# Kernel tuning notes

Hardware: AMD Instinct MI355X
Metric: run time of the kernel (lower is better)

The kernel has to match this reference:

```python
import jax, jax.numpy as jnp
import numpy as np

B, N, K, D, V, L = 16, 512, 16, 256, 64, 2


def setup_inputs() -> dict:
    key = jax.random.key(0)
    ks = jax.random.split(key, 20)
    inp = {
        "node_reps": jax.random.normal(ks[0], (B, N, D), dtype=jnp.float32),
        "mask": jax.random.uniform(ks[1], (B, N), dtype=jnp.float32),
        "in_indices": jax.random.randint(ks[2], (B, N, K), 0, N),
        "in_edges": jax.random.randint(ks[3], (B, N, K), 0, V),
        "in_mask": jax.random.uniform(ks[4], (B, N, K), dtype=jnp.float32),
        "out_indices": jax.random.randint(ks[5], (B, N, K), 0, N),
        "out_edges": jax.random.randint(ks[6], (B, N, K), 0, V),
        "out_mask": jax.random.uniform(ks[7], (B, N, K), dtype=jnp.float32),
        "edge_emb": jax.random.normal(ks[8], (V, D), dtype=jnp.float32) * 0.02,
        # packed gate weights, order [ig, fg, og, cell] along last dim
        "Wi": jax.random.normal(ks[9], (2 * D, 4 * D), dtype=jnp.float32) * 0.02,
        "Wo": jax.random.normal(ks[10], (2 * D, 4 * D), dtype=jnp.float32) * 0.02,
        "Ui": jax.random.normal(ks[11], (2 * D, 4 * D), dtype=jnp.float32) * 0.02,
        "Uo": jax.random.normal(ks[12], (2 * D, 4 * D), dtype=jnp.float32) * 0.02,
        "bi": jnp.zeros((4 * D,), dtype=jnp.float32),
        "bo": jnp.zeros((4 * D,), dtype=jnp.float32),
        "bui": jnp.zeros((4 * D,), dtype=jnp.float32),
        "buo": jnp.zeros((4 * D,), dtype=jnp.float32),
    }
    return inp


def _agg(h, idx, edge_reps, nmask):
    # gather neighbor states: [B,N,K,D]
    neigh = h[jnp.arange(h.shape[0])[:, None, None], idx]
    x = jnp.concatenate([neigh, edge_reps], axis=-1) * nmask[..., None]
    return x.sum(axis=2)  # [B,N,2D]


def reference(node_reps, mask, in_indices, in_edges, in_mask,
              out_indices, out_edges, out_mask,
              edge_emb, Wi, Wo, Ui, Uo, bi, bo, bui, buo):
    in_edge_reps = edge_emb[in_edges]    # [B,N,K,D]
    out_edge_reps = edge_emb[out_edges]  # [B,N,K,D]

    in_reps = _agg(node_reps, in_indices, in_edge_reps, in_mask)     # [B,N,2D]
    out_reps = _agg(node_reps, out_indices, out_edge_reps, out_mask)  # [B,N,2D]
    z_static = in_reps @ Wi + bi + out_reps @ Wo + bo  # [B,N,4D]

    h = node_reps
    c = jnp.zeros_like(node_reps)
    reps = []
    for _ in range(L):
        in_pre = _agg(h, in_indices, in_edge_reps, in_mask)
        out_pre = _agg(h, out_indices, out_edge_reps, out_mask)
        z = z_static + in_pre @ Ui + bui + out_pre @ Uo + buo  # [B,N,4D]
        ig, fg, og, ci = jnp.split(z, 4, axis=-1)
        ig = jax.nn.sigmoid(ig)
        fg = jax.nn.sigmoid(fg)
        og = jax.nn.sigmoid(og)
        ci = jnp.tanh(ci)
        c_new = fg * c + ig * ci
        h_new = og * jnp.tanh(c_new)
        c = c_new * mask[..., None]
        h = h_new * mask[..., None]
        reps.append(h)
    return (jnp.stack(reps, axis=0), h, c)
```

## Files before the change

### kernel.cpp

```cpp
#include <hip/hip_runtime.h>
#include <math.h>

#define Kn 16
#define Dd 256
#define NC 1024
#define XS 640
#define MR 8192

typedef _Float16 h8 __attribute__((ext_vector_type(8)));
typedef _Float16 h4 __attribute__((ext_vector_type(4)));
typedef _Float16 h2 __attribute__((ext_vector_type(2)));
typedef float f4 __attribute__((ext_vector_type(4)));

__device__ __forceinline__ void gload16(_Float16* lds, const _Float16* g) {
  __builtin_amdgcn_global_load_lds(
      (const __attribute__((address_space(1))) void*)g,
      (__attribute__((address_space(3))) void*)lds, 16, 0, 0);
}

__device__ __forceinline__ float fsigm(float x) { return 1.f / (1.f + __expf(-x)); }
__device__ __forceinline__ float ftanh(float x) { return 2.f / (1.f + __expf(-2.f * x)) - 1.f; }

__global__ __launch_bounds__(256, 4) void mega2_kernel(
    const float* __restrict__ node_reps, const float* __restrict__ emb,
    const int* __restrict__ iidx, const float* __restrict__ im,
    const int* __restrict__ oidx, const float* __restrict__ om,
    const int* __restrict__ ie, const int* __restrict__ oe,
    const float* __restrict__ Wi, const float* __restrict__ Wo,
    const float* __restrict__ Ui, const float* __restrict__ Uo,
    const float* __restrict__ bi, const float* __restrict__ bo,
    const float* __restrict__ bui, const float* __restrict__ buo,
    _Float16* __restrict__ X, _Float16* __restrict__ W0f,
    _Float16* __restrict__ Wlf, float* __restrict__ biasq) {
  __shared__ __align__(16) char smem[20480];
  const int b = blockIdx.x, t = threadIdx.x;

  if (b < 2048) {
    const int lane = t & 63;
    const int wid = t >> 6;
    const int row = (b & 7) * 1024 + (b >> 3) * 4 + wid;
    const int half = lane >> 5;
    const int lc = lane & 31;
    const int sel = lane >> 4, p16 = lane & 15;

    const int bb = row * Kn + p16;
    const int* ap = (sel == 0)   ? (iidx + bb)
                    : (sel == 1) ? ((const int*)im + bb)
                    : (sel == 2) ? (oidx + bb)
                                 : ((const int*)om + bb);
    const int cmb = *ap;
    const int cmbe = *(((lane & 16) ? oe : ie) + bb);

    const int hb = row & ~511;
    const float* hp = node_reps + ((size_t)hb << 8) + (lc << 3);

    float acc[8] = {};
#pragma unroll
    for (int kb = 0; kb < 2; kb++) {
      f4 w0[8], w1[8];
#pragma unroll
      for (int k = 0; k < 8; k++) {
        const int ik = __shfl(cmb, (lane & 32) | (kb * 8 + k), 64);
        const float* p = hp + ((size_t)ik << 8);
        w0[k] = *(const f4*)p;
        w1[k] = *(const f4*)(p + 4);
      }
      __builtin_amdgcn_sched_barrier(0);
#pragma unroll
      for (int k = 0; k < 8; k++) {
        const float mk = __int_as_float(__shfl(cmb, (lane & 32) | 16 | (kb * 8 + k), 64));
#pragma unroll
        for (int c = 0; c < 4; c++) {
          acc[c] += mk * w0[k][c];
          acc[4 + c] += mk * w1[k][c];
        }
      }
    }

    {
      float b0 = 0.f, b1 = 0.f;
      const int vmine = 2 * lane - half * 64;
#pragma unroll
      for (int k = 0; k < 16; k++) {
        const int ec = __shfl(cmbe, (half << 4) | k, 64);
        const float mc = __int_as_float(__shfl(cmb, (lane & 32) | 16 | k, 64));
        b0 += (ec == vmine) ? mc : 0.f;
        b1 += (ec == vmine + 1) ? mc : 0.f;
      }
      h2 bp;
      bp[0] = (_Float16)b0;
      bp[1] = (_Float16)b1;
      *(h2*)&X[(size_t)row * XS + 512 + lane * 2] = bp;
    }

    h8 o;
#pragma unroll
    for (int c = 0; c < 8; c++) o[c] = (_Float16)acc[c];
    *(h8*)&X[(size_t)row * XS + half * 256 + lc * 8] = o;
  } else if (b < 2176) {
    float* seT = (float*)smem;
    float* sa = (float*)(smem + 4096);
    const int pb = b - 2048;
    const int vgrp = pb >> 2, cq = pb & 3;
    const int dir = vgrp >> 4;
    const int v0 = (vgrp & 15) * 4;
    const float* Wa = dir ? Wo : Wi;
    const float* Ua = dir ? Uo : Ui;
#pragma unroll
    for (int r = 0; r < 4; r++) seT[t * 4 + r] = emb[(v0 + r) * 256 + t];
    __syncthreads();

    const int l = t & 63, ds = t >> 6;
    const int cp0 = cq * 256 + l * 4;
    const int g = (cp0 >> 4) & 3;
    const int d0 = ((cp0 >> 6) << 4) + (cp0 & 15);
    const int c0 = g * 256 + d0;
    const float* wp = Wa + (size_t)(256 + ds * 64) * NC + c0;
    const float* up = Ua + (size_t)(256 + ds * 64) * NC + c0;
    const float* sT = seT + (ds * 64) * 4;

    f4 av[4] = {};
    for (int bb8 = 0; bb8 < 8; bb8++) {
      f4 wv8[8], uv8[8];
#pragma unroll
      for (int ii = 0; ii < 8; ii++) {
        const int dd = bb8 * 8 + ii;
        wv8[ii] = *(const f4*)(wp + (size_t)dd * NC);
        uv8[ii] = *(const f4*)(up + (size_t)dd * NC);
      }
      __builtin_amdgcn_sched_barrier(0);
#pragma unroll
      for (int ii = 0; ii < 8; ii++) {
        const int dd = bb8 * 8 + ii;
        const f4 wv = wv8[ii] + uv8[ii];
        const f4 s0 = *(const f4*)&sT[dd * 4];
        av[0] += s0[0] * wv;
        av[1] += s0[1] * wv;
        av[2] += s0[2] * wv;
        av[3] += s0[3] * wv;
      }
    }
#pragma unroll
    for (int r = 0; r < 4; r++) *(f4*)&sa[((ds * 4 + r) * 64 + l) * 4] = av[r];
    __syncthreads();
    {
      const int r = t >> 6, fl = t & 63;
      f4 s = {0.f, 0.f, 0.f, 0.f};
#pragma unroll
      for (int d = 0; d < 4; d++) s += *(const f4*)&sa[((d * 4 + r) * 64 + fl) * 4];
      const int vvg = vgrp * 4 + r;
      const int kt = 16 + (vvg >> 5);
      const int lhi = (vvg >> 3) & 3;
      const int j = vvg & 7;
      const int cpb = cq * 256 + fl * 4;
#pragma unroll
      for (int i = 0; i < 4; i++) {
        const int cp = cpb + i;
        W0f[kt * 32768 + (cp >> 4) * 512 + (lhi * 16 + (cp & 15)) * 8 + j] = (_Float16)s[i];
      }
    }
  } else if (b < 2208) {
    const int p = b - 2176;
    const int kk = t >> 3;
    const int tc = t & 7;
    const int k = (p & 15) * 32 + kk;
    const float* rowp;
    const float* rowp2 = nullptr;
    if (p < 16) {
      rowp  = (k < 256) ? Wi + (size_t)k * NC : Wo + (size_t)(k - 256) * NC;
      rowp2 = (k < 256) ? Ui + (size_t)k * NC : Uo + (size_t)(k - 256) * NC;
    } else {
      rowp  = (k < 256) ? Ui + (size_t)k * NC : Uo + (size_t)(k - 256) * NC;
    }
    _Float16* dst = (p < 16) ? (W0f + p * 32768) : (Wlf + (p - 16) * 32768);
    const int lane0 = (kk >> 3) * 16;
    const int j = kk & 7;
    for (int bb8 = 0; bb8 < 4; bb8++) {
      f4 w8[8], u8[8];
#pragma unroll
      for (int ii = 0; ii < 8; ii++) {
        const int c = (bb8 * 8 + ii) * 32 + tc * 4;
        w8[ii] = *(const f4*)(rowp + c);
        if (p < 16) u8[ii] = *(const f4*)(rowp2 + c);
      }
      __builtin_amdgcn_sched_barrier(0);
#pragma unroll
      for (int ii = 0; ii < 8; ii++) {
        const int c = (bb8 * 8 + ii) * 32 + tc * 4;
        const int g = c >> 8, d = c & 255;
        const int nt = 4 * (d >> 4) + g;
        const int lb = lane0 + (d & 15);
        f4 v = w8[ii];
        if (p < 16) v += u8[ii];
#pragma unroll
        for (int q = 0; q < 4; q++)
          dst[nt * 512 + (lb + q) * 8 + j] = (_Float16)v[q];
      }
    }
  } else {
#pragma unroll
    for (int i = 0; i < 4; i++) {
      const int cq = t * 4 + i;
      const int dd = cq >> 2, g = cq & 3;
      const int c = g * 256 + dd;
      biasq[cq] = bi[c] + bo[c] + bui[c] + buo[c];
    }
  }
}

__global__ __launch_bounds__(256, 4) void agg_kernel(
    const _Float16* __restrict__ src,
    const int* __restrict__ iidx, const float* __restrict__ im,
    const int* __restrict__ oidx, const float* __restrict__ om,
    _Float16* __restrict__ X) {
  const int lane = threadIdx.x & 63;
  const int wid = threadIdx.x >> 6;
  const int b = blockIdx.x;
  const int row = (b & 7) * 1024 + (b >> 3) * 4 + wid;
  const int half = lane >> 5;
  const int lc = lane & 31;
  const int sel = lane >> 4, p16 = lane & 15;

  const int bb = row * Kn + p16;
  const int* ap = (sel == 0)   ? (iidx + bb)
                  : (sel == 1) ? ((const int*)im + bb)
                  : (sel == 2) ? (oidx + bb)
                               : ((const int*)om + bb);
  const int cmb = *ap;

  const int hb = row & ~511;
  const _Float16* hp = src + ((size_t)hb << 8) + (lc << 3);
  _Float16* xp = &X[(size_t)row * XS + half * 256 + lc * 8];

  const h8 xold = *(const h8*)xp;

  h8 w[16];
#pragma unroll
  for (int k = 0; k < 16; k++) {
    const int ik = __shfl(cmb, (lane & 32) | k, 64);
    w[k] = *(const h8*)(hp + ((size_t)ik << 8));
  }
  __builtin_amdgcn_sched_barrier(0);

  float acc[8] = {};
#pragma unroll
  for (int k = 0; k < 16; k++) {
    const float mk = __int_as_float(__shfl(cmb, (lane & 32) | 16 | k, 64));
#pragma unroll
    for (int c = 0; c < 8; c++) acc[c] += mk * (float)w[k][c];
  }

  h8 o;
#pragma unroll
  for (int c = 0; c < 8; c++) o[c] = (_Float16)(acc[c] - (float)xold[c]);
  *(h8*)xp = o;
}

template <bool WITH_Z>
__global__ __launch_bounds__(512) void fused_gemm(
    const _Float16* __restrict__ A, const _Float16* __restrict__ Wf,
    const float* __restrict__ biasq, _Float16* __restrict__ zq,
    const float* __restrict__ mask,
    float* __restrict__ reps, float* __restrict__ hbuf,
    _Float16* __restrict__ h16, float* __restrict__ cbuf) {
  constexpr int KT = WITH_Z ? 20 : 16;
  constexpr int D = 2;
  __shared__ __align__(16) _Float16 lds[3][8192];

  const int wg = (blockIdx.x & 7) * 64 + (blockIdx.x >> 3);
  const int bm = wg >> 3, bn = wg & 7;
  const int tid = threadIdx.x, lane = tid & 63, wid = tid >> 6;
  const int wr = wid >> 1, wc = wid & 1;
  const int lr = lane & 15, lg = lane >> 4;

  f4 acc[2][4] = {};

  const _Float16* srcA0 = A + (size_t)(bm * 128 + wid * 16 + lr) * XS + lg * 8;
  const _Float16* srcB0 = Wf + ((size_t)bn * 8 + wid) * 512 + lane * 8;
  const int woff = wid * 512;

  auto stage = [&](int buf, int kt) {
    _Float16* base = lds[buf];
    gload16(base + woff, srcA0 + kt * 32);
    gload16(base + 4096 + woff, srcB0 + (size_t)kt * 32768);
  };

  stage(0, 0);
  stage(1, 1);
  asm volatile("s_waitcnt vmcnt(%0)" :: "i"(D) : "memory");
  __builtin_amdgcn_s_barrier();

  int cur = 0;
  for (int kt = 0; kt < KT; kt++) {
    if (kt + 2 < KT) stage(cur == 0 ? 2 : cur - 1, kt + 2);

    const _Float16* base = lds[cur];
    h8 a[2], bfr[4];
#pragma unroll
    for (int m = 0; m < 2; m++) a[m] = *(const h8*)&base[(wr * 2 + m) * 512 + lane * 8];
#pragma unroll
    for (int n = 0; n < 4; n++) bfr[n] = *(const h8*)&base[4096 + (wc * 4 + n) * 512 + lane * 8];
    asm volatile("s_waitcnt lgkmcnt(0)" ::: "memory");
    __builtin_amdgcn_sched_barrier(0);

    __builtin_amdgcn_s_setprio(1);
#pragma unroll
    for (int m = 0; m < 2; m++)
#pragma unroll
      for (int n = 0; n < 4; n++)
        acc[m][n] = __builtin_amdgcn_mfma_f32_16x16x32_f16(a[m], bfr[n], acc[m][n], 0, 0, 0);
    __builtin_amdgcn_s_setprio(0);

    if (kt + 2 < KT) asm volatile("s_waitcnt vmcnt(%0)" :: "i"(D) : "memory");
    else             asm volatile("s_waitcnt vmcnt(0)" ::: "memory");
    __builtin_amdgcn_sched_barrier(0);
    __builtin_amdgcn_s_barrier();

    cur = (cur == 2) ? 0 : cur + 1;
  }

  const int d = (bn * 2 + wc) * 16 + lr;
  const int row0 = bm * 128 + wr * 32;
  f4 bq = {0.f, 0.f, 0.f, 0.f};
  if (WITH_Z) bq = *(const f4*)&biasq[d * 4];
#pragma unroll
  for (int i = 0; i < 2; i++) {
#pragma unroll
    for (int r = 0; r < 4; r++) {
      const int row = row0 + i * 16 + lg * 4 + r;
      const size_t off = (size_t)row * Dd + d;
      const float mk = mask[row];
      float zi, zf, zo, zc, cold;
      if (WITH_Z) {
        zi = acc[i][0][r] + bq.x;
        zf = acc[i][1][r] + bq.y;
        zo = acc[i][2][r] + bq.z;
        zc = acc[i][3][r] + bq.w;
        h4 oz;
        oz[0] = (_Float16)zi; oz[1] = (_Float16)zf;
        oz[2] = (_Float16)zo; oz[3] = (_Float16)zc;
        *(h4*)&zq[off * 4] = oz;
        cold = 0.f;
      } else {
        const h4 zb = *(const h4*)&zq[off * 4];
        zi = (float)zb[0] + acc[i][0][r];
        zf = (float)zb[1] + acc[i][1][r];
        zo = (float)zb[2] + acc[i][2][r];
        zc = (float)zb[3] + acc[i][3][r];
        cold = fsigm((float)zb[0]) * ftanh((float)zb[3]) * mk;
      }
      const float ig = fsigm(zi), fg = fsigm(zf), og = fsigm(zo), ci = ftanh(zc);
      const float cn = fg * cold + ig * ci;
      const float hn = og * ftanh(cn);
      const float hm = hn * mk;
      if (WITH_Z) {
        __builtin_nontemporal_store(hm, &reps[off]);
        h16[off] = (_Float16)hm;
      } else {
        __builtin_nontemporal_store(hm, &reps[off]);
        __builtin_nontemporal_store(hm, &hbuf[off]);
        __builtin_nontemporal_store(cn * mk, &cbuf[off]);
      }
    }
  }
}

extern "C" void kernel_launch(void* const* d_in, const int* in_sizes, int n_in,
                              void* d_out, int out_size, void* d_ws, size_t ws_size,
                              hipStream_t stream) {
  const float* node_reps = (const float*)d_in[0];
  const float* mask      = (const float*)d_in[1];
  const int*   in_idx    = (const int*)d_in[2];
  const int*   in_edges  = (const int*)d_in[3];
  const float* in_mask   = (const float*)d_in[4];
  const int*   out_idx   = (const int*)d_in[5];
  const int*   out_edges = (const int*)d_in[6];
  const float* out_mask  = (const float*)d_in[7];
  const float* edge_emb  = (const float*)d_in[8];
  const float* Wi  = (const float*)d_in[9];
  const float* Wo  = (const float*)d_in[10];
  const float* Ui  = (const float*)d_in[11];
  const float* Uo  = (const float*)d_in[12];
  const float* bi  = (const float*)d_in[13];
  const float* bo  = (const float*)d_in[14];
  const float* bui = (const float*)d_in[15];
  const float* buo = (const float*)d_in[16];

  float* out = (float*)d_out;
  const size_t MD = (size_t)MR * Dd;
  float* reps0 = out;
  float* reps1 = out + MD;
  float* hbuf  = out + 2 * MD;
  float* cbuf  = out + 3 * MD;

  _Float16* X    = (_Float16*)d_ws;
  _Float16* zq   = X + (size_t)MR * XS;
  _Float16* W0f  = zq + (size_t)MR * NC;
  _Float16* Wlf  = W0f + 640 * 1024;
  _Float16* h16  = Wlf + 512 * 1024;
  float*    biasq = (float*)(h16 + (size_t)MR * Dd);

  mega2_kernel<<<2209, 256, 0, stream>>>(node_reps, edge_emb, in_idx, in_mask,
                                         out_idx, out_mask, in_edges, out_edges,
                                         Wi, Wo, Ui, Uo, bi, bo, bui, buo,
                                         X, W0f, Wlf, biasq);
  fused_gemm<true><<<512, 512, 0, stream>>>(
      X, W0f, biasq, zq, mask, reps0, nullptr, h16, nullptr);
  agg_kernel<<<2048, 256, 0, stream>>>(h16, in_idx, in_mask, out_idx, out_mask, X);
  fused_gemm<false><<<512, 512, 0, stream>>>(
      X, Wlf, nullptr, zq, mask, reps1, hbuf, nullptr, cbuf);
}
```

Baseline: 72.20 us.

## Convert node_reps to fp16 up front and split first aggregation into own kernel

The weight-packing work and an fp32-to-fp16 conversion of node_reps now run in a small prep kernel. The first-layer neighbor aggregation becomes a separate kernel that gathers fp16 rows, with all 16 neighbor loads issued at once. This halves the bytes read by the random-access gather, but adds one kernel launch, an extra full pass over node_reps, and a serialization point. Aggregation inputs are also rounded to fp16 before summation.

```diff
diff --git a/kernel.cpp b/kernel.cpp
--- a/kernel.cpp
+++ b/kernel.cpp
@@ -21,87 +21,21 @@
 __device__ __forceinline__ float fsigm(float x) { return 1.f / (1.f + __expf(-x)); }
 __device__ __forceinline__ float ftanh(float x) { return 2.f / (1.f + __expf(-2.f * x)) - 1.f; }
 
-__global__ __launch_bounds__(256, 4) void mega2_kernel(
+__global__ __launch_bounds__(256) void prep_kernel(
     const float* __restrict__ node_reps, const float* __restrict__ emb,
-    const int* __restrict__ iidx, const float* __restrict__ im,
-    const int* __restrict__ oidx, const float* __restrict__ om,
-    const int* __restrict__ ie, const int* __restrict__ oe,
     const float* __restrict__ Wi, const float* __restrict__ Wo,
     const float* __restrict__ Ui, const float* __restrict__ Uo,
     const float* __restrict__ bi, const float* __restrict__ bo,
     const float* __restrict__ bui, const float* __restrict__ buo,
-    _Float16* __restrict__ X, _Float16* __restrict__ W0f,
-    _Float16* __restrict__ Wlf, float* __restrict__ biasq) {
+    _Float16* __restrict__ W0f, _Float16* __restrict__ Wlf,
+    float* __restrict__ biasq, _Float16* __restrict__ n16) {
   __shared__ __align__(16) char smem[20480];
   const int b = blockIdx.x, t = threadIdx.x;
 
-  if (b < 2048) {
-    const int lane = t & 63;
-    const int wid = t >> 6;
-    const int row = (b & 7) * 1024 + (b >> 3) * 4 + wid;
-    const int half = lane >> 5;
-    const int lc = lane & 31;
-    const int sel = lane >> 4, p16 = lane & 15;
-
-    const int bb = row * Kn + p16;
-    const int* ap = (sel == 0)   ? (iidx + bb)
-                    : (sel == 1) ? ((const int*)im + bb)
-                    : (sel == 2) ? (oidx + bb)
-                                 : ((const int*)om + bb);
-    const int cmb = *ap;
-    const int cmbe = *(((lane & 16) ? oe : ie) + bb);
-
-    const int hb = row & ~511;
-    const float* hp = node_reps + ((size_t)hb << 8) + (lc << 3);
-
-    float acc[8] = {};
-#pragma unroll
-    for (int kb = 0; kb < 2; kb++) {
-      f4 w0[8], w1[8];
-#pragma unroll
-      for (int k = 0; k < 8; k++) {
-        const int ik = __shfl(cmb, (lane & 32) | (kb * 8 + k), 64);
-        const float* p = hp + ((size_t)ik << 8);
-        w0[k] = *(const f4*)p;
-        w1[k] = *(const f4*)(p + 4);
-      }
-      __builtin_amdgcn_sched_barrier(0);
-#pragma unroll
-      for (int k = 0; k < 8; k++) {
-        const float mk = __int_as_float(__shfl(cmb, (lane & 32) | 16 | (kb * 8 + k), 64));
-#pragma unroll
-        for (int c = 0; c < 4; c++) {
-          acc[c] += mk * w0[k][c];
-          acc[4 + c] += mk * w1[k][c];
-        }
-      }
-    }
-
-    {
-      float b0 = 0.f, b1 = 0.f;
-      const int vmine = 2 * lane - half * 64;
-#pragma unroll
-      for (int k = 0; k < 16; k++) {
-        const int ec = __shfl(cmbe, (half << 4) | k, 64);
-        const float mc = __int_as_float(__shfl(cmb, (lane & 32) | 16 | k, 64));
-        b0 += (ec == vmine) ? mc : 0.f;
-        b1 += (ec == vmine + 1) ? mc : 0.f;
-      }
-      h2 bp;
-      bp[0] = (_Float16)b0;
-      bp[1] = (_Float16)b1;
-      *(h2*)&X[(size_t)row * XS + 512 + lane * 2] = bp;
-    }
-
-    h8 o;
-#pragma unroll
-    for (int c = 0; c < 8; c++) o[c] = (_Float16)acc[c];
-    *(h8*)&X[(size_t)row * XS + half * 256 + lc * 8] = o;
-  } else if (b < 2176) {
+  if (b < 128) {
     float* seT = (float*)smem;
     float* sa = (float*)(smem + 4096);
-    const int pb = b - 2048;
-    const int vgrp = pb >> 2, cq = pb & 3;
+    const int vgrp = b >> 2, cq = b & 3;
     const int dir = vgrp >> 4;
     const int v0 = (vgrp & 15) * 4;
     const float* Wa = dir ? Wo : Wi;
@@ -159,8 +93,8 @@
         W0f[kt * 32768 + (cp >> 4) * 512 + (lhi * 16 + (cp & 15)) * 8 + j] = (_Float16)s[i];
       }
     }
-  } else if (b < 2208) {
-    const int p = b - 2176;
+  } else if (b < 160) {
+    const int p = b - 128;
     const int kk = t >> 3;
     const int tc = t & 7;
     const int k = (p & 15) * 32 + kk;
@@ -197,7 +131,7 @@
           dst[nt * 512 + (lb + q) * 8 + j] = (_Float16)v[q];
       }
     }
-  } else {
+  } else if (b == 160) {
 #pragma unroll
     for (int i = 0; i < 4; i++) {
       const int cq = t * 4 + i;
@@ -205,10 +139,85 @@
       const int c = g * 256 + dd;
       biasq[cq] = bi[c] + bo[c] + bui[c] + buo[c];
     }
-  }
-}
-
-__global__ __launch_bounds__(256, 4) void agg_kernel(
+  } else {
+    const int cb = b - 161;
+#pragma unroll
+    for (int r = 0; r < 8; r++) {
+      const int off = cb * 16384 + r * 2048 + t * 8;
+      const f4 v0 = *(const f4*)(node_reps + off);
+      const f4 v1 = *(const f4*)(node_reps + off + 4);
+      h8 o;
+#pragma unroll
+      for (int jj = 0; jj < 4; jj++) { o[jj] = (_Float16)v0[jj]; o[jj + 4] = (_Float16)v1[jj]; }
+      *(h8*)&n16[off] = o;
+    }
+  }
+}
+
+__global__ __launch_bounds__(256, 4) void agg0_kernel(
+    const _Float16* __restrict__ n16,
+    const int* __restrict__ iidx, const float* __restrict__ im,
+    const int* __restrict__ oidx, const float* __restrict__ om,
+    const int* __restrict__ ie, const int* __restrict__ oe,
+    _Float16* __restrict__ X) {
+  const int lane = threadIdx.x & 63;
+  const int wid = threadIdx.x >> 6;
+  const int b = blockIdx.x;
+  const int row = (b & 7) * 1024 + (b >> 3) * 4 + wid;
+  const int half = lane >> 5;
+  const int lc = lane & 31;
+  const int sel = lane >> 4, p16 = lane & 15;
+
+  const int bb = row * Kn + p16;
+  const int* ap = (sel == 0)   ? (iidx + bb)
+                  : (sel == 1) ? ((const int*)im + bb)
+                  : (sel == 2) ? (oidx + bb)
+                               : ((const int*)om + bb);
+  const int cmb = *ap;
+  const int cmbe = *(((lane & 16) ? oe : ie) + bb);
+
+  const int hb = row & ~511;
+  const _Float16* hp = n16 + ((size_t)hb << 8) + (lc << 3);
+
+  h8 w[16];
+#pragma unroll
+  for (int k = 0; k < 16; k++) {
+    const int ik = __shfl(cmb, (lane & 32) | k, 64);
+    w[k] = *(const h8*)(hp + ((size_t)ik << 8));
+  }
+  __builtin_amdgcn_sched_barrier(0);
+
+  float acc[8] = {};
+#pragma unroll
+  for (int k = 0; k < 16; k++) {
+    const float mk = __int_as_float(__shfl(cmb, (lane & 32) | 16 | k, 64));
+#pragma unroll
+    for (int c = 0; c < 8; c++) acc[c] += mk * (float)w[k][c];
+  }
+
+  {
+    float b0 = 0.f, b1 = 0.f;
+    const int vmine = 2 * lane - half * 64;
+#pragma unroll
+    for (int k = 0; k < 16; k++) {
+      const int ec = __shfl(cmbe, (half << 4) | k, 64);
+      const float mc = __int_as_float(__shfl(cmb, (lane & 32) | 16 | k, 64));
+      b0 += (ec == vmine) ? mc : 0.f;
+      b1 += (ec == vmine + 1) ? mc : 0.f;
+    }
+    h2 bp;
+    bp[0] = (_Float16)b0;
+    bp[1] = (_Float16)b1;
+    *(h2*)&X[(size_t)row * XS + 512 + lane * 2] = bp;
+  }
+
+  h8 o;
+#pragma unroll
+  for (int c = 0; c < 8; c++) o[c] = (_Float16)acc[c];
+  *(h8*)&X[(size_t)row * XS + half * 256 + lc * 8] = o;
+}
+
+__global__ __launch_bounds__(256, 4) void agg1_kernel(
     const _Float16* __restrict__ src,
     const int* __restrict__ iidx, const float* __restrict__ im,
     const int* __restrict__ oidx, const float* __restrict__ om,
@@ -397,16 +406,17 @@
   _Float16* zq   = X + (size_t)MR * XS;
   _Float16* W0f  = zq + (size_t)MR * NC;
   _Float16* Wlf  = W0f + 640 * 1024;
-  _Float16* h16  = Wlf + 512 * 1024;
+  _Float16* n16  = Wlf + 512 * 1024;
+  _Float16* h16  = n16 + (size_t)MR * Dd;
   float*    biasq = (float*)(h16 + (size_t)MR * Dd);
 
-  mega2_kernel<<<2209, 256, 0, stream>>>(node_reps, edge_emb, in_idx, in_mask,
-                                         out_idx, out_mask, in_edges, out_edges,
-                                         Wi, Wo, Ui, Uo, bi, bo, bui, buo,
-                                         X, W0f, Wlf, biasq);
+  prep_kernel<<<289, 256, 0, stream>>>(node_reps, edge_emb, Wi, Wo, Ui, Uo,
+                                       bi, bo, bui, buo, W0f, Wlf, biasq, n16);
+  agg0_kernel<<<2048, 256, 0, stream>>>(n16, in_idx, in_mask, out_idx, out_mask,
+                                        in_edges, out_edges, X);
   fused_gemm<true><<<512, 512, 0, stream>>>(
       X, W0f, biasq, zq, mask, reps0, nullptr, h16, nullptr);
-  agg_kernel<<<2048, 256, 0, stream>>>(h16, in_idx, in_mask, out_idx, out_mask, X);
+  agg1_kernel<<<2048, 256, 0, stream>>>(h16, in_idx, in_mask, out_idx, out_mask, X);
   fused_gemm<false><<<512, 512, 0, stream>>>(
       X, Wlf, nullptr, zq, mask, reps1, hbuf, nullptr, cbuf);
 }
```

Result: no change. 72.75 us, median of 2 (+0.8%).
